# Performance work log

Hardware: AMD Instinct MI355X
Metric: run time of the kernel (lower is better)

## Reference

```python
import jax, jax.numpy as jnp
import numpy as np

K = 8  # search_range in sample_wise_recolor
BIG = 1e30


def setup_inputs() -> dict:
    key = jax.random.key(0)
    ks = jax.random.split(key, 6)
    L, N = 16384, 10000  # L: upsampled candidate voxels (multiple of 8), N: target points
    pred_F = jax.random.normal(ks[0], (L,), jnp.float32)
    cand_xyz = jax.random.normal(ks[1], (L, 3), jnp.float32) * 50.0
    cand_rgb = jax.random.uniform(ks[2], (L, 3), jnp.float32)
    tgt_xyz = jax.random.normal(ks[3], (N, 3), jnp.float32) * 50.0
    tgt_rgb = jax.random.uniform(ks[4], (N, 3), jnp.float32)
    keep_target = jax.random.randint(ks[5], (L,), 0, 2, jnp.int32)
    return {"pred_F": pred_F, "cand_xyz": cand_xyz, "cand_rgb": cand_rgb,
            "tgt_xyz": tgt_xyz, "tgt_rgb": tgt_rgb, "keep_target": keep_target,
            "points_num": 8192}


def _get_keep(pred, points_num):
    # local-max mask over groups of 8 children (scatter of per-row argmax)
    L = pred.shape[0]
    p8 = pred.reshape(-1, 8)
    rows = jnp.arange(p8.shape[0])
    is_local_max = jnp.zeros(p8.shape, dtype=bool).at[rows, jnp.argmax(p8, axis=1)].set(True).reshape(-1)
    # kthvalue over the non-local-max subset: local-max entries pushed to +inf so the
    # k-th smallest of the full sorted array equals the k-th smallest of the subset.
    k = L - points_num  # static python int
    vals = jnp.where(is_local_max, jnp.inf, pred)
    threshold = jnp.sort(vals)[k - 1]
    return (pred > threshold) | is_local_max


def _pairwise_sqdist(a, b):
    # a: [P,3], b: [Q,3] -> [P,Q] squared distances
    a2 = jnp.sum(a * a, axis=1)
    b2 = jnp.sum(b * b, axis=1)
    d2 = a2[:, None] + b2[None, :] - 2.0 * (a @ b.T)
    return jnp.maximum(d2, 0.0)


def _recolor_loss(cand_xyz, rgb, keep, tgt_xyz, tgt_rgb):
    L = cand_xyz.shape[0]
    N = tgt_xyz.shape[0]
    d2 = _pairwise_sqdist(tgt_xyz, cand_xyz)  # [N, L]

    # ---- recolor_backward: KNN from each target point into kept candidates ----
    d_masked = jnp.where(keep[None, :], d2, BIG)
    neg_d, idx = jax.lax.top_k(-d_masked, K)  # [N, K]
    d = -neg_d
    zero_mask = d == 0.0
    min_mask = (d == jnp.min(d, axis=1, keepdims=True)) & ~jnp.any(zero_mask, axis=1)[:, None]
    w = jnp.where(min_mask, 1.0 / jnp.sqrt(jnp.maximum(d, 1e-30)), 0.0)  # [N, K]

    flat_idx = idx.reshape(-1)
    num = jnp.zeros((L, 3), rgb.dtype).at[flat_idx].add((tgt_rgb[:, None, :] * w[:, :, None]).reshape(-1, 3))
    den = jnp.zeros((L,), rgb.dtype).at[flat_idx].add(w.reshape(-1))
    has_den = den != 0.0
    recolored = jnp.where(has_den[:, None], num / jnp.where(has_den, den, 1.0)[:, None], 0.0)

    # exact-match (zero-distance) targets overwrite; scatter with safe out-of-range dummy row
    safe_idx = jnp.where(zero_mask, idx, L).reshape(-1)
    tgt_exp = jnp.broadcast_to(tgt_rgb[:, None, :], (N, K, 3)).reshape(-1, 3)
    recolored = jnp.concatenate([recolored, jnp.zeros((1, 3), rgb.dtype)], 0).at[safe_idx].set(tgt_exp)[:L]
    empty = jnp.concatenate([~has_den, jnp.zeros((1,), bool)], 0).at[safe_idx].set(False)[:L]
    empty = empty & keep  # only kept candidates matter

    # ---- recolor_forward: kept candidates with no color yet pull from nearest targets ----
    neg_df, idxf = jax.lax.top_k(-d2.T, K)  # [L, K]
    df = -neg_df
    mf = df == jnp.min(df, axis=1, keepdims=True)
    rec_fwd = jnp.sum(tgt_rgb[idxf] * mf[:, :, None], axis=1) / jnp.sum(mf, axis=1, keepdims=True).astype(rgb.dtype)
    recolored = jnp.where(empty[:, None], rec_fwd, recolored)

    # L1 loss over kept candidates only; recolor target is no-grad in the original
    recolored = jax.lax.stop_gradient(recolored)
    return jnp.sum(jnp.where(keep[:, None], jnp.abs(rgb - recolored), 0.0))


def reference(pred_F, cand_xyz, cand_rgb, tgt_xyz, tgt_rgb, keep_target, points_num):
    keep = _get_keep(jax.lax.stop_gradient(pred_F), points_num)  # @torch.no_grad
    # coord recon loss: BCE-with-logits, reduction='sum'
    t = keep_target.astype(pred_F.dtype)
    coord_loss = jnp.sum(jnp.maximum(pred_F, 0.0) - pred_F * t + jnp.log1p(jnp.exp(-jnp.abs(pred_F))))
    # inverse_transform_for_color in training mode: x * 255
    rgb = cand_rgb * 255.0
    rgb_loss = _recolor_loss(cand_xyz, rgb, keep, tgt_xyz, tgt_rgb)
    return jnp.stack([coord_loss, rgb_loss])
```

## Files before the change

kernel.cpp:

```cpp
#include <hip/hip_runtime.h>
#include <hip/hip_bf16.h>


#define SCAN_T 256
#define BCH 512
#define FCH 512

__global__ __launch_bounds__(256) void k_init(
    const float* __restrict__ txyz, float4* __restrict__ ttile,
    float4* __restrict__ numden, int* __restrict__ zerohit,
    unsigned long long* __restrict__ tmin, unsigned long long* __restrict__ fmin,
    unsigned int* __restrict__ ghist, int* __restrict__ counters,
    float* __restrict__ out, int L, int N) {
  int i = blockIdx.x * 256 + threadIdx.x;
  if (i < N) {
    float x = txyz[3*i], y = txyz[3*i+1], z = txyz[3*i+2];
    ttile[i] = make_float4(x, y, z, fmaf(x, x, fmaf(y, y, z * z)));
    tmin[i] = ~0ull;
  }
  if (i < L) {
    numden[i] = make_float4(0.f, 0.f, 0.f, 0.f);
    zerohit[i] = 0;
    fmin[i] = ~0ull;
  }
  if (i < 2048) ghist[i] = 0u;
  if (i < 8) counters[i] = 0;
  if (i < 2) out[i] = 0.f;
}

__global__ __launch_bounds__(256) void k_prep(
    const float* __restrict__ pred, unsigned int* __restrict__ key,
    unsigned char* __restrict__ islm, unsigned int* __restrict__ ghist, int L) {
  __shared__ float sp[256];
  __shared__ unsigned char fl[256];
  __shared__ unsigned int lh[2048];
  int tid = threadIdx.x;
  int i = blockIdx.x * 256 + tid;
  sp[tid] = (i < L) ? pred[i] : -3e38f;
  fl[tid] = 0;
  for (int b = tid; b < 2048; b += 256) lh[b] = 0u;
  __syncthreads();
  if (tid < 32) {
    int base = tid * 8;
    float bv = sp[base]; int bi = 0;
    #pragma unroll
    for (int j = 1; j < 8; ++j) {
      float v = sp[base + j];
      if (v > bv) { bv = v; bi = j; }
    }
    fl[base + bi] = 1;
  }
  __syncthreads();
  if (i < L) {
    unsigned char lm = fl[tid];
    unsigned int fb = __float_as_uint(sp[tid]);
    unsigned int k = lm ? 0xFF800000u
                        : ((fb & 0x80000000u) ? ~fb : (fb | 0x80000000u));
    key[i] = k;
    islm[i] = lm;
    atomicAdd(&lh[k >> 21], 1u);
  }
  __syncthreads();
  for (int b = tid; b < 2048; b += 256) {
    unsigned int c = lh[b];
    if (c) atomicAdd(&ghist[b], c);
  }
}

__global__ __launch_bounds__(256) void k_sel(
    const unsigned int* __restrict__ key, const unsigned int* __restrict__ ghist,
    const int* __restrict__ pnum_p, float* __restrict__ thr_out, int L) {
  __shared__ unsigned int buf[16384];
  __shared__ unsigned int hist[256];
  __shared__ unsigned int sB, sR, sM;
  int tid = threadIdx.x;
  unsigned int rank = (unsigned int)(L - pnum_p[0] - 1);
  if (tid == 0) sM = 0u;
  if (tid < 64) {
    unsigned int sum = 0;
    #pragma unroll 4
    for (int j = 0; j < 32; ++j) sum += ghist[tid * 32 + j];
    unsigned int incl = sum;
    for (int o = 1; o < 64; o <<= 1) {
      unsigned int v = __shfl_up(incl, o);
      if (tid >= o) incl += v;
    }
    unsigned int excl = incl - sum;
    bool cond = (rank >= excl) && (rank < incl);
    unsigned long long bal = __ballot(cond);
    int first = __ffsll((long long)bal) - 1;
    if (tid == first) {
      unsigned int r = rank - excl, cum = 0;
      for (int j = 0; j < 32; ++j) {
        unsigned int c = ghist[tid * 32 + j];
        if (r < cum + c) { sB = (unsigned int)(tid * 32 + j); sR = r - cum; break; }
        cum += c;
      }
    }
  }
  __syncthreads();
  unsigned int B = sB;
  for (int i = tid; i < L; i += 256) {
    unsigned int k = key[i];
    if ((k >> 21) == B) { unsigned int p = atomicAdd(&sM, 1u); buf[p] = k; }
  }
  __syncthreads();
  unsigned int M = sM;
  unsigned int pfx = B << 21;
  const int shifts[3] = {13, 5, 0};
  const unsigned int masks[3] = {0xFFE00000u, 0xFFFFE000u, 0xFFFFFFE0u};
  const int nbs[3] = {256, 256, 32};
  for (int p = 0; p < 3; ++p) {
    hist[tid & 255] = 0u;
    __syncthreads();
    unsigned int mk = masks[p]; int sh = shifts[p]; int nb = nbs[p];
    unsigned int pm = pfx & mk;
    for (unsigned int j = tid; j < M; j += 256) {
      unsigned int k = buf[j];
      if ((k & mk) == pm) atomicAdd(&hist[(k >> sh) & (unsigned)(nb - 1)], 1u);
    }
    __syncthreads();
    if (tid < 64) {
      int g = nb >> 6; if (g < 1) g = 1;
      unsigned int sum = 0;
      for (int j = 0; j < g; ++j) {
        int idx = tid * g + j;
        if (idx < nb) sum += hist[idx];
      }
      unsigned int incl = sum;
      for (int o = 1; o < 64; o <<= 1) {
        unsigned int v = __shfl_up(incl, o);
        if (tid >= o) incl += v;
      }
      unsigned int excl = incl - sum;
      unsigned int r = sR;
      bool cond = (r >= excl) && (r < incl);
      unsigned long long bal = __ballot(cond);
      int first = __ffsll((long long)bal) - 1;
      if (tid == first) {
        unsigned int rr = r - excl, cum = 0;
        for (int j = 0; j < g; ++j) {
          int idx = tid * g + j;
          if (idx >= nb) break;
          unsigned int c = hist[idx];
          if (rr < cum + c) { sB = (unsigned int)idx; sR = rr - cum; break; }
          cum += c;
        }
      }
    }
    __syncthreads();
    pfx |= sB << sh;
    __syncthreads();
  }
  if (tid == 0) {
    unsigned int kk = pfx;
    unsigned int fb = (kk & 0x80000000u) ? (kk & 0x7FFFFFFFu) : ~kk;
    thr_out[0] = __uint_as_float(fb);
  }
}

__global__ __launch_bounds__(256) void k_keepc(
    const float* __restrict__ pred, const unsigned char* __restrict__ islm,
    const float* __restrict__ thr_p, const float* __restrict__ cxyz,
    const int* __restrict__ ktgt, int* __restrict__ keep,
    float4* __restrict__ klist, int* __restrict__ kidx,
    int* __restrict__ counters, float* __restrict__ out, int L) {
  int i = blockIdx.x * 256 + threadIdx.x;
  float thr = thr_p[0];
  float term = 0.f;
  if (i < L) {
    float p = pred[i];
    bool kp = (p > thr) || islm[i];
    keep[i] = kp ? 1 : 0;
    if (kp) {
      int pos = atomicAdd(&counters[0], 1);
      float x = cxyz[3*i], y = cxyz[3*i+1], z = cxyz[3*i+2];
      klist[pos] = make_float4(x, y, z, fmaf(x, x, fmaf(y, y, z * z)));
      kidx[pos] = i;
    }
    float t = (float)ktgt[i];
    term = fmaxf(p, 0.f) - p * t + log1pf(expf(-fabsf(p)));
  }
  for (int off = 32; off > 0; off >>= 1) term += __shfl_down(term, off);
  if ((threadIdx.x & 63) == 0) atomicAdd(&out[0], term);
}

__global__ __launch_bounds__(SCAN_T) void k_bwd(
    const float* __restrict__ txyz, const float4* __restrict__ klist,
    const int* __restrict__ kidx, const int* __restrict__ counters,
    unsigned long long* __restrict__ tmin, int N) {
  int kc = counters[0];
  int c0 = blockIdx.y * BCH;
  if (c0 >= kc) return;
  int c1 = min(c0 + BCH, kc);
  __shared__ float4 sc[SCAN_T];
  int tid = threadIdx.x;
  int t = blockIdx.x * SCAN_T + tid;
  float tx = 0.f, ty = 0.f, tz = 0.f;
  if (t < N) { tx = txyz[3*t]; ty = txyz[3*t+1]; tz = txyz[3*t+2]; }
  float ntx = -2.f * tx, nty = -2.f * ty, ntz = -2.f * tz;
  float best = 3e38f; int bpos = -1;
  for (int tile = c0; tile < c1; tile += SCAN_T) {
    int cnt = min(SCAN_T, c1 - tile);
    if (tid < cnt) sc[tid] = klist[tile + tid];
    __syncthreads();
    #pragma unroll 8
    for (int c = 0; c < cnt; ++c) {
      float4 cd = sc[c];
      float d = fmaf(ntx, cd.x, cd.w);
      d = fmaf(nty, cd.y, d);
      d = fmaf(ntz, cd.z, d);
      if (d < best) { best = d; bpos = tile + c; }
    }
    __syncthreads();
  }
  if (t < N && bpos >= 0) {
    float4 cd = klist[bpos];
    float dx = tx - cd.x, dy = ty - cd.y, dz = tz - cd.z;
    float dtrue = fmaf(dx, dx, fmaf(dy, dy, dz * dz));
    unsigned long long pack =
        ((unsigned long long)__float_as_uint(dtrue) << 32) |
        (unsigned int)kidx[bpos];
    atomicMin(&tmin[t], pack);
  }
}

__global__ __launch_bounds__(256) void k_bwd_scatter(
    const float* __restrict__ trgb, const unsigned long long* __restrict__ tmin,
    float4* __restrict__ numden, int* __restrict__ zerohit,
    float4* __restrict__ zcolor, int N) {
  int t = blockIdx.x * 256 + threadIdx.x;
  if (t >= N) return;
  unsigned long long pack = tmin[t];
  float d = __uint_as_float((unsigned int)(pack >> 32));
  int idx = (int)(pack & 0xFFFFFFFFull);
  float r = trgb[3*t], g = trgb[3*t+1], b = trgb[3*t+2];
  if (d == 0.0f) {
    zerohit[idx] = 1;
    zcolor[idx] = make_float4(r, g, b, 0.f);
  } else {
    float w = 1.0f / sqrtf(fmaxf(d, 1e-30f));
    atomicAdd(&numden[idx].x, r * w);
    atomicAdd(&numden[idx].y, g * w);
    atomicAdd(&numden[idx].z, b * w);
    atomicAdd(&numden[idx].w, w);
  }
}

__global__ __launch_bounds__(256) void k_empty(
    const int* __restrict__ keep, const float4* __restrict__ numden,
    const int* __restrict__ zerohit, int* __restrict__ elist,
    int* __restrict__ counters, int L) {
  int l = blockIdx.x * 256 + threadIdx.x;
  if (l < L && keep[l] && (numden[l].w == 0.f) && (zerohit[l] == 0)) {
    int pos = atomicAdd(&counters[1], 1);
    elist[pos] = l;
  }
}

__global__ __launch_bounds__(SCAN_T) void k_fwd(
    const float4* __restrict__ ttile, const float* __restrict__ cxyz,
    const int* __restrict__ elist, const int* __restrict__ counters,
    unsigned long long* __restrict__ fmin, int N) {
  int ec = counters[1];
  if ((int)(blockIdx.x * SCAN_T) >= ec) return;
  __shared__ float4 st[SCAN_T];
  int tid = threadIdx.x;
  int e = blockIdx.x * SCAN_T + tid;
  bool act = e < ec;
  int l = act ? elist[e] : 0;
  float cx = 0.f, cy = 0.f, cz = 0.f;
  if (act) { cx = cxyz[3*l]; cy = cxyz[3*l+1]; cz = cxyz[3*l+2]; }
  float ncx = -2.f * cx, ncy = -2.f * cy, ncz = -2.f * cz;
  float c2 = fmaf(cx, cx, fmaf(cy, cy, cz * cz));
  int t0 = blockIdx.y * FCH;
  int t1 = min(t0 + FCH, N);
  float best = 3e38f; int bidx = 0;
  for (int tile = t0; tile < t1; tile += SCAN_T) {
    int cnt = min(SCAN_T, t1 - tile);
    if (tid < cnt) st[tid] = ttile[tile + tid];
    __syncthreads();
    #pragma unroll 8
    for (int c = 0; c < cnt; ++c) {
      float4 td = st[c];
      float d = fmaf(ncx, td.x, td.w);
      d = fmaf(ncy, td.y, d);
      d = fmaf(ncz, td.z, d);
      if (d < best) { best = d; bidx = tile + c; }
    }
    __syncthreads();
  }
  if (act) {
    float dkey = fmaxf(best + c2, 0.f);
    unsigned long long pack =
        ((unsigned long long)__float_as_uint(dkey) << 32) | (unsigned int)bidx;
    atomicMin(&fmin[l], pack);
  }
}

__global__ __launch_bounds__(256) void k_loss(
    const float* __restrict__ crgb, const float* __restrict__ trgb,
    const int* __restrict__ keep, const float4* __restrict__ numden,
    const int* __restrict__ zerohit, const float4* __restrict__ zcolor,
    const unsigned long long* __restrict__ fmin,
    float* __restrict__ out, int L) {
  int l = blockIdx.x * 256 + threadIdx.x;
  float loss = 0.f;
  if (l < L && keep[l]) {
    float rr, rg, rb;
    if (zerohit[l]) {
      float4 z = zcolor[l]; rr = z.x; rg = z.y; rb = z.z;
    } else {
      float4 nd = numden[l];
      if (nd.w != 0.f) { rr = nd.x / nd.w; rg = nd.y / nd.w; rb = nd.z / nd.w; }
      else {
        int ti = (int)(fmin[l] & 0xFFFFFFFFull);
        rr = trgb[3*ti]; rg = trgb[3*ti+1]; rb = trgb[3*ti+2];
      }
    }
    float sr = crgb[3*l] * 255.f, sg = crgb[3*l+1] * 255.f, sb = crgb[3*l+2] * 255.f;
    loss = fabsf(sr - rr) + fabsf(sg - rg) + fabsf(sb - rb);
  }
  for (int off = 32; off > 0; off >>= 1) loss += __shfl_down(loss, off);
  if ((threadIdx.x & 63) == 0) atomicAdd(&out[1], loss);
}

extern "C" void kernel_launch(void* const* d_in, const int* in_sizes, int n_in,
                              void* d_out, int out_size, void* d_ws, size_t ws_size,
                              hipStream_t stream) {
  const float* pred = (const float*)d_in[0];
  const float* cxyz = (const float*)d_in[1];
  const float* crgb = (const float*)d_in[2];
  const float* txyz = (const float*)d_in[3];
  const float* trgb = (const float*)d_in[4];
  const int*   ktgt = (const int*)d_in[5];
  const int*   pnum = (const int*)d_in[6];
  int L = in_sizes[0];
  int N = in_sizes[3] / 3;

  char* ws = (char*)d_ws;
  size_t off = 0;
  int* keep = (int*)(ws + off);                      off += (size_t)L * 4;
  float4* klist = (float4*)(ws + off);               off += (size_t)L * 16;
  int* kidx = (int*)(ws + off);                      off += (size_t)L * 4;
  float4* ttile = (float4*)(ws + off);               off += (size_t)((N + 3) & ~3) * 16;
  float4* numden = (float4*)(ws + off);              off += (size_t)L * 16;
  int* zerohit = (int*)(ws + off);                   off += (size_t)L * 4;
  float4* zcolor = (float4*)(ws + off);              off += (size_t)L * 16;
  unsigned long long* tmin = (unsigned long long*)(ws + off); off += (size_t)((N + 1) & ~1) * 8;
  unsigned long long* fmin = (unsigned long long*)(ws + off); off += (size_t)L * 8;
  int* elist = (int*)(ws + off);                     off += (size_t)L * 4;
  unsigned int* key = (unsigned int*)(ws + off);     off += (size_t)L * 4;
  unsigned char* islm = (unsigned char*)(ws + off);  off += ((size_t)L + 15) & ~15ull;
  unsigned int* ghist = (unsigned int*)(ws + off);   off += 2048 * 4;
  float* thr_slot = (float*)(ws + off);              off += 16;
  int* counters = (int*)(ws + off);                  off += 256;

  float* out = (float*)d_out;
  int mx = max(L, N);
  int nbL = (L + 255) / 256;

  k_init<<<(mx + 255) / 256, 256, 0, stream>>>(
      txyz, ttile, numden, zerohit, tmin, fmin, ghist, counters, out, L, N);

  k_prep<<<nbL, 256, 0, stream>>>(pred, key, islm, ghist, L);

  k_sel<<<1, 256, 0, stream>>>(key, ghist, pnum, thr_slot, L);

  k_keepc<<<nbL, 256, 0, stream>>>(
      pred, islm, thr_slot, cxyz, ktgt, keep, klist, kidx, counters, out, L);

  dim3 g2((N + SCAN_T - 1) / SCAN_T, (L + BCH - 1) / BCH);
  k_bwd<<<g2, SCAN_T, 0, stream>>>(txyz, klist, kidx, counters, tmin, N);

  k_bwd_scatter<<<(N + 255) / 256, 256, 0, stream>>>(
      trgb, tmin, numden, zerohit, zcolor, N);

  k_empty<<<nbL, 256, 0, stream>>>(keep, numden, zerohit, elist, counters, L);

  dim3 g3((L + SCAN_T - 1) / SCAN_T, (N + FCH - 1) / FCH);
  k_fwd<<<g3, SCAN_T, 0, stream>>>(ttile, cxyz, elist, counters, fmin, N);

  k_loss<<<(L + 255) / 256, 256, 0, stream>>>(
      crgb, trgb, keep, numden, zerohit, zcolor, fmin, out, L);
}
```

Measured before the change: 164.2 us.

## Fuse all pipeline stages into one cooperative persistent kernel with grid syncs

Replaces the nine separate kernel launches with a single cooperative kernel of 256 blocks that moves between stages using grid.sync(). This removes per-launch overhead and inter-kernel gaps. It also vectorizes the local-max and key preparation to one thread per group of 8 with global histogram atomics, parallelizes the radix-select bucket gather across the grid, and splits the NN scans into fixed chunk tasks. The cost is reduced parallelism in the scan phases, since only 256 blocks run, plus the latency of each grid barrier. Contention on global atomics also rises because the block-local histogram is gone.

```diff
diff --git a/kernel.cpp b/kernel.cpp
--- a/kernel.cpp
+++ b/kernel.cpp
@@ -1,89 +1,82 @@
 #include <hip/hip_runtime.h>
+#include <hip/hip_cooperative_groups.h>
 #include <hip/hip_bf16.h>
 
-
-#define SCAN_T 256
-#define BCH 512
-#define FCH 512
-
-__global__ __launch_bounds__(256) void k_init(
-    const float* __restrict__ txyz, float4* __restrict__ ttile,
-    float4* __restrict__ numden, int* __restrict__ zerohit,
-    unsigned long long* __restrict__ tmin, unsigned long long* __restrict__ fmin,
-    unsigned int* __restrict__ ghist, int* __restrict__ counters,
-    float* __restrict__ out, int L, int N) {
-  int i = blockIdx.x * 256 + threadIdx.x;
-  if (i < N) {
-    float x = txyz[3*i], y = txyz[3*i+1], z = txyz[3*i+2];
-    ttile[i] = make_float4(x, y, z, fmaf(x, x, fmaf(y, y, z * z)));
-    tmin[i] = ~0ull;
-  }
-  if (i < L) {
-    numden[i] = make_float4(0.f, 0.f, 0.f, 0.f);
-    zerohit[i] = 0;
-    fmin[i] = ~0ull;
-  }
-  if (i < 2048) ghist[i] = 0u;
-  if (i < 8) counters[i] = 0;
-  if (i < 2) out[i] = 0.f;
-}
-
-__global__ __launch_bounds__(256) void k_prep(
-    const float* __restrict__ pred, unsigned int* __restrict__ key,
-    unsigned char* __restrict__ islm, unsigned int* __restrict__ ghist, int L) {
-  __shared__ float sp[256];
-  __shared__ unsigned char fl[256];
-  __shared__ unsigned int lh[2048];
-  int tid = threadIdx.x;
-  int i = blockIdx.x * 256 + tid;
-  sp[tid] = (i < L) ? pred[i] : -3e38f;
-  fl[tid] = 0;
-  for (int b = tid; b < 2048; b += 256) lh[b] = 0u;
-  __syncthreads();
-  if (tid < 32) {
-    int base = tid * 8;
-    float bv = sp[base]; int bi = 0;
+namespace cg = cooperative_groups;
+
+
+#define NBLK 256
+#define NTHR 256
+
+struct Params {
+  const float* pred; const float* cxyz; const float* crgb;
+  const float* txyz; const float* trgb; const int* ktgt; const int* pnum;
+  float4* klist; float4* ttile; float4* numden; float4* zcolor;
+  unsigned long long* tmin; unsigned long long* fmin;
+  int* keep; int* kidx; int* zerohit; int* elist;
+  unsigned int* key; unsigned int* ghist; unsigned int* gbuf;
+  float* thr_slot; int* counters; unsigned char* islm;
+  float* out; int L; int N;
+};
+
+__global__ __launch_bounds__(NTHR, 1) void k_all(Params p) {
+  cg::grid_group grid = cg::this_grid();
+  __shared__ float4 tile[256];
+  __shared__ unsigned int hist[256];
+  __shared__ unsigned int buf[16384];
+  __shared__ unsigned int sB, sR;
+  int tid = threadIdx.x, bid = blockIdx.x;
+  int gidx = bid * NTHR + tid;
+  int gsz = (int)gridDim.x * NTHR;
+  int L = p.L, N = p.N;
+
+  for (int i = gidx; i < N; i += gsz) {
+    float x = p.txyz[3*i], y = p.txyz[3*i+1], z = p.txyz[3*i+2];
+    p.ttile[i] = make_float4(x, y, z, fmaf(x, x, fmaf(y, y, z * z)));
+    p.tmin[i] = ~0ull;
+  }
+  for (int i = gidx; i < L; i += gsz) {
+    p.numden[i] = make_float4(0.f, 0.f, 0.f, 0.f);
+    p.zerohit[i] = 0;
+    p.fmin[i] = ~0ull;
+  }
+  if (gidx < 2048) p.ghist[gidx] = 0u;
+  if (gidx < 8) p.counters[gidx] = 0;
+  if (gidx < 2) p.out[gidx] = 0.f;
+  grid.sync();
+
+  int ngroups = L >> 3;
+  for (int g = gidx; g < ngroups; g += gsz) {
+    const float4* pv = (const float4*)p.pred + (size_t)g * 2;
+    float4 a = pv[0], b = pv[1];
+    float v[8] = {a.x, a.y, a.z, a.w, b.x, b.y, b.z, b.w};
+    int bi = 0; float bv = v[0];
     #pragma unroll
-    for (int j = 1; j < 8; ++j) {
-      float v = sp[base + j];
-      if (v > bv) { bv = v; bi = j; }
-    }
-    fl[base + bi] = 1;
-  }
-  __syncthreads();
-  if (i < L) {
-    unsigned char lm = fl[tid];
-    unsigned int fb = __float_as_uint(sp[tid]);
-    unsigned int k = lm ? 0xFF800000u
-                        : ((fb & 0x80000000u) ? ~fb : (fb | 0x80000000u));
-    key[i] = k;
-    islm[i] = lm;
-    atomicAdd(&lh[k >> 21], 1u);
-  }
-  __syncthreads();
-  for (int b = tid; b < 2048; b += 256) {
-    unsigned int c = lh[b];
-    if (c) atomicAdd(&ghist[b], c);
-  }
-}
-
-__global__ __launch_bounds__(256) void k_sel(
-    const unsigned int* __restrict__ key, const unsigned int* __restrict__ ghist,
-    const int* __restrict__ pnum_p, float* __restrict__ thr_out, int L) {
-  __shared__ unsigned int buf[16384];
-  __shared__ unsigned int hist[256];
-  __shared__ unsigned int sB, sR, sM;
-  int tid = threadIdx.x;
-  unsigned int rank = (unsigned int)(L - pnum_p[0] - 1);
-  if (tid == 0) sM = 0u;
+    for (int j = 1; j < 8; ++j) if (v[j] > bv) { bv = v[j]; bi = j; }
+    unsigned int kk[8];
+    unsigned long long lmpack = 0ull;
+    #pragma unroll
+    for (int j = 0; j < 8; ++j) {
+      unsigned int fb = __float_as_uint(v[j]);
+      unsigned int mk = (fb & 0x80000000u) ? ~fb : (fb | 0x80000000u);
+      if (j == bi) { mk = 0xFF800000u; lmpack |= 1ull << (8 * j); }
+      kk[j] = mk;
+      atomicAdd(&p.ghist[mk >> 21], 1u);
+    }
+    ((uint4*)p.key)[g*2]   = make_uint4(kk[0], kk[1], kk[2], kk[3]);
+    ((uint4*)p.key)[g*2+1] = make_uint4(kk[4], kk[5], kk[6], kk[7]);
+    *(unsigned long long*)(p.islm + (size_t)g * 8) = lmpack;
+  }
+  grid.sync();
+
+  unsigned int rank = (unsigned int)(L - p.pnum[0] - 1);
   if (tid < 64) {
     unsigned int sum = 0;
-    #pragma unroll 4
-    for (int j = 0; j < 32; ++j) sum += ghist[tid * 32 + j];
+    for (int j = 0; j < 32; ++j) sum += p.ghist[tid * 32 + j];
     unsigned int incl = sum;
     for (int o = 1; o < 64; o <<= 1) {
-      unsigned int v = __shfl_up(incl, o);
-      if (tid >= o) incl += v;
+      unsigned int vv = __shfl_up(incl, o);
+      if (tid >= o) incl += vv;
     }
     unsigned int excl = incl - sum;
     bool cond = (rank >= excl) && (rank < incl);
@@ -92,7 +85,7 @@
     if (tid == first) {
       unsigned int r = rank - excl, cum = 0;
       for (int j = 0; j < 32; ++j) {
-        unsigned int c = ghist[tid * 32 + j];
+        unsigned int c = p.ghist[tid * 32 + j];
         if (r < cum + c) { sB = (unsigned int)(tid * 32 + j); sR = r - cum; break; }
         cum += c;
       }
@@ -100,287 +93,256 @@
   }
   __syncthreads();
   unsigned int B = sB;
-  for (int i = tid; i < L; i += 256) {
-    unsigned int k = key[i];
-    if ((k >> 21) == B) { unsigned int p = atomicAdd(&sM, 1u); buf[p] = k; }
-  }
-  __syncthreads();
-  unsigned int M = sM;
-  unsigned int pfx = B << 21;
-  const int shifts[3] = {13, 5, 0};
-  const unsigned int masks[3] = {0xFFE00000u, 0xFFFFE000u, 0xFFFFFFE0u};
-  const int nbs[3] = {256, 256, 32};
-  for (int p = 0; p < 3; ++p) {
-    hist[tid & 255] = 0u;
+  for (int i = gidx; i < L; i += gsz) {
+    unsigned int k = p.key[i];
+    if ((k >> 21) == B) {
+      unsigned int pos = atomicAdd((unsigned int*)&p.counters[2], 1u);
+      p.gbuf[pos] = k;
+    }
+  }
+  grid.sync();
+
+  if (bid == 0) {
+    unsigned int M = (unsigned int)p.counters[2];
+    for (unsigned int j = tid; j < M; j += NTHR) buf[j] = p.gbuf[j];
     __syncthreads();
-    unsigned int mk = masks[p]; int sh = shifts[p]; int nb = nbs[p];
-    unsigned int pm = pfx & mk;
-    for (unsigned int j = tid; j < M; j += 256) {
-      unsigned int k = buf[j];
-      if ((k & mk) == pm) atomicAdd(&hist[(k >> sh) & (unsigned)(nb - 1)], 1u);
-    }
-    __syncthreads();
-    if (tid < 64) {
-      int g = nb >> 6; if (g < 1) g = 1;
-      unsigned int sum = 0;
-      for (int j = 0; j < g; ++j) {
-        int idx = tid * g + j;
-        if (idx < nb) sum += hist[idx];
-      }
-      unsigned int incl = sum;
-      for (int o = 1; o < 64; o <<= 1) {
-        unsigned int v = __shfl_up(incl, o);
-        if (tid >= o) incl += v;
-      }
-      unsigned int excl = incl - sum;
-      unsigned int r = sR;
-      bool cond = (r >= excl) && (r < incl);
-      unsigned long long bal = __ballot(cond);
-      int first = __ffsll((long long)bal) - 1;
-      if (tid == first) {
-        unsigned int rr = r - excl, cum = 0;
-        for (int j = 0; j < g; ++j) {
-          int idx = tid * g + j;
-          if (idx >= nb) break;
-          unsigned int c = hist[idx];
-          if (rr < cum + c) { sB = (unsigned int)idx; sR = rr - cum; break; }
-          cum += c;
-        }
-      }
-    }
-    __syncthreads();
-    pfx |= sB << sh;
-    __syncthreads();
-  }
-  if (tid == 0) {
-    unsigned int kk = pfx;
-    unsigned int fb = (kk & 0x80000000u) ? (kk & 0x7FFFFFFFu) : ~kk;
-    thr_out[0] = __uint_as_float(fb);
-  }
-}
-
-__global__ __launch_bounds__(256) void k_keepc(
-    const float* __restrict__ pred, const unsigned char* __restrict__ islm,
-    const float* __restrict__ thr_p, const float* __restrict__ cxyz,
-    const int* __restrict__ ktgt, int* __restrict__ keep,
-    float4* __restrict__ klist, int* __restrict__ kidx,
-    int* __restrict__ counters, float* __restrict__ out, int L) {
-  int i = blockIdx.x * 256 + threadIdx.x;
-  float thr = thr_p[0];
-  float term = 0.f;
-  if (i < L) {
-    float p = pred[i];
-    bool kp = (p > thr) || islm[i];
-    keep[i] = kp ? 1 : 0;
-    if (kp) {
-      int pos = atomicAdd(&counters[0], 1);
-      float x = cxyz[3*i], y = cxyz[3*i+1], z = cxyz[3*i+2];
-      klist[pos] = make_float4(x, y, z, fmaf(x, x, fmaf(y, y, z * z)));
-      kidx[pos] = i;
-    }
-    float t = (float)ktgt[i];
-    term = fmaxf(p, 0.f) - p * t + log1pf(expf(-fabsf(p)));
-  }
-  for (int off = 32; off > 0; off >>= 1) term += __shfl_down(term, off);
-  if ((threadIdx.x & 63) == 0) atomicAdd(&out[0], term);
-}
-
-__global__ __launch_bounds__(SCAN_T) void k_bwd(
-    const float* __restrict__ txyz, const float4* __restrict__ klist,
-    const int* __restrict__ kidx, const int* __restrict__ counters,
-    unsigned long long* __restrict__ tmin, int N) {
-  int kc = counters[0];
-  int c0 = blockIdx.y * BCH;
-  if (c0 >= kc) return;
-  int c1 = min(c0 + BCH, kc);
-  __shared__ float4 sc[SCAN_T];
-  int tid = threadIdx.x;
-  int t = blockIdx.x * SCAN_T + tid;
-  float tx = 0.f, ty = 0.f, tz = 0.f;
-  if (t < N) { tx = txyz[3*t]; ty = txyz[3*t+1]; tz = txyz[3*t+2]; }
-  float ntx = -2.f * tx, nty = -2.f * ty, ntz = -2.f * tz;
-  float best = 3e38f; int bpos = -1;
-  for (int tile = c0; tile < c1; tile += SCAN_T) {
-    int cnt = min(SCAN_T, c1 - tile);
-    if (tid < cnt) sc[tid] = klist[tile + tid];
-    __syncthreads();
-    #pragma unroll 8
-    for (int c = 0; c < cnt; ++c) {
-      float4 cd = sc[c];
-      float d = fmaf(ntx, cd.x, cd.w);
-      d = fmaf(nty, cd.y, d);
-      d = fmaf(ntz, cd.z, d);
-      if (d < best) { best = d; bpos = tile + c; }
-    }
-    __syncthreads();
-  }
-  if (t < N && bpos >= 0) {
-    float4 cd = klist[bpos];
-    float dx = tx - cd.x, dy = ty - cd.y, dz = tz - cd.z;
-    float dtrue = fmaf(dx, dx, fmaf(dy, dy, dz * dz));
-    unsigned long long pack =
-        ((unsigned long long)__float_as_uint(dtrue) << 32) |
-        (unsigned int)kidx[bpos];
-    atomicMin(&tmin[t], pack);
-  }
-}
-
-__global__ __launch_bounds__(256) void k_bwd_scatter(
-    const float* __restrict__ trgb, const unsigned long long* __restrict__ tmin,
-    float4* __restrict__ numden, int* __restrict__ zerohit,
-    float4* __restrict__ zcolor, int N) {
-  int t = blockIdx.x * 256 + threadIdx.x;
-  if (t >= N) return;
-  unsigned long long pack = tmin[t];
-  float d = __uint_as_float((unsigned int)(pack >> 32));
-  int idx = (int)(pack & 0xFFFFFFFFull);
-  float r = trgb[3*t], g = trgb[3*t+1], b = trgb[3*t+2];
-  if (d == 0.0f) {
-    zerohit[idx] = 1;
-    zcolor[idx] = make_float4(r, g, b, 0.f);
-  } else {
-    float w = 1.0f / sqrtf(fmaxf(d, 1e-30f));
-    atomicAdd(&numden[idx].x, r * w);
-    atomicAdd(&numden[idx].y, g * w);
-    atomicAdd(&numden[idx].z, b * w);
-    atomicAdd(&numden[idx].w, w);
-  }
-}
-
-__global__ __launch_bounds__(256) void k_empty(
-    const int* __restrict__ keep, const float4* __restrict__ numden,
-    const int* __restrict__ zerohit, int* __restrict__ elist,
-    int* __restrict__ counters, int L) {
-  int l = blockIdx.x * 256 + threadIdx.x;
-  if (l < L && keep[l] && (numden[l].w == 0.f) && (zerohit[l] == 0)) {
-    int pos = atomicAdd(&counters[1], 1);
-    elist[pos] = l;
-  }
-}
-
-__global__ __launch_bounds__(SCAN_T) void k_fwd(
-    const float4* __restrict__ ttile, const float* __restrict__ cxyz,
-    const int* __restrict__ elist, const int* __restrict__ counters,
-    unsigned long long* __restrict__ fmin, int N) {
-  int ec = counters[1];
-  if ((int)(blockIdx.x * SCAN_T) >= ec) return;
-  __shared__ float4 st[SCAN_T];
-  int tid = threadIdx.x;
-  int e = blockIdx.x * SCAN_T + tid;
-  bool act = e < ec;
-  int l = act ? elist[e] : 0;
-  float cx = 0.f, cy = 0.f, cz = 0.f;
-  if (act) { cx = cxyz[3*l]; cy = cxyz[3*l+1]; cz = cxyz[3*l+2]; }
-  float ncx = -2.f * cx, ncy = -2.f * cy, ncz = -2.f * cz;
-  float c2 = fmaf(cx, cx, fmaf(cy, cy, cz * cz));
-  int t0 = blockIdx.y * FCH;
-  int t1 = min(t0 + FCH, N);
-  float best = 3e38f; int bidx = 0;
-  for (int tile = t0; tile < t1; tile += SCAN_T) {
-    int cnt = min(SCAN_T, t1 - tile);
-    if (tid < cnt) st[tid] = ttile[tile + tid];
-    __syncthreads();
-    #pragma unroll 8
-    for (int c = 0; c < cnt; ++c) {
-      float4 td = st[c];
-      float d = fmaf(ncx, td.x, td.w);
-      d = fmaf(ncy, td.y, d);
-      d = fmaf(ncz, td.z, d);
-      if (d < best) { best = d; bidx = tile + c; }
-    }
-    __syncthreads();
-  }
-  if (act) {
-    float dkey = fmaxf(best + c2, 0.f);
-    unsigned long long pack =
-        ((unsigned long long)__float_as_uint(dkey) << 32) | (unsigned int)bidx;
-    atomicMin(&fmin[l], pack);
-  }
-}
-
-__global__ __launch_bounds__(256) void k_loss(
-    const float* __restrict__ crgb, const float* __restrict__ trgb,
-    const int* __restrict__ keep, const float4* __restrict__ numden,
-    const int* __restrict__ zerohit, const float4* __restrict__ zcolor,
-    const unsigned long long* __restrict__ fmin,
-    float* __restrict__ out, int L) {
-  int l = blockIdx.x * 256 + threadIdx.x;
-  float loss = 0.f;
-  if (l < L && keep[l]) {
-    float rr, rg, rb;
-    if (zerohit[l]) {
-      float4 z = zcolor[l]; rr = z.x; rg = z.y; rb = z.z;
+    unsigned int pfx = B << 21;
+    const int shifts[3] = {13, 5, 0};
+    const unsigned int masks[3] = {0xFFE00000u, 0xFFFFE000u, 0xFFFFFFE0u};
+    const int nbs[3] = {256, 256, 32};
+    for (int pass = 0; pass < 3; ++pass) {
+      hist[tid] = 0u;
+      __syncthreads();
+      unsigned int mk = masks[pass]; int sh = shifts[pass]; int nb = nbs[pass];
+      unsigned int pm = pfx & mk;
+      for (unsigned int j = tid; j < M; j += NTHR) {
+        unsigned int k = buf[j];
+        if ((k & mk) == pm) atomicAdd(&hist[(k >> sh) & (unsigned)(nb - 1)], 1u);
+      }
+      __syncthreads();
+      if (tid < 64) {
+        int g = nb >> 6; if (g < 1) g = 1;
+        unsigned int sum = 0;
+        for (int j = 0; j < g; ++j) { int idx = tid * g + j; if (idx < nb) sum += hist[idx]; }
+        unsigned int incl = sum;
+        for (int o = 1; o < 64; o <<= 1) {
+          unsigned int vv = __shfl_up(incl, o);
+          if (tid >= o) incl += vv;
+        }
+        unsigned int excl = incl - sum;
+        unsigned int r = sR;
+        bool cond = (r >= excl) && (r < incl);
+        unsigned long long bal = __ballot(cond);
+        int first = __ffsll((long long)bal) - 1;
+        if (tid == first) {
+          unsigned int rr = r - excl, cum = 0;
+          for (int j = 0; j < g; ++j) {
+            int idx = tid * g + j; if (idx >= nb) break;
+            unsigned int c = hist[idx];
+            if (rr < cum + c) { sB = (unsigned int)idx; sR = rr - cum; break; }
+            cum += c;
+          }
+        }
+      }
+      __syncthreads();
+      pfx |= sB << sh;
+      __syncthreads();
+    }
+    if (tid == 0) {
+      unsigned int kk2 = pfx;
+      unsigned int fb = (kk2 & 0x80000000u) ? (kk2 & 0x7FFFFFFFu) : ~kk2;
+      p.thr_slot[0] = __uint_as_float(fb);
+    }
+  }
+  grid.sync();
+
+  {
+    float thr = p.thr_slot[0];
+    float term = 0.f;
+    for (int i = gidx; i < L; i += gsz) {
+      float v = p.pred[i];
+      bool kp = (v > thr) || p.islm[i];
+      p.keep[i] = kp ? 1 : 0;
+      if (kp) {
+        int pos = atomicAdd(&p.counters[0], 1);
+        float x = p.cxyz[3*i], y = p.cxyz[3*i+1], z = p.cxyz[3*i+2];
+        p.klist[pos] = make_float4(x, y, z, fmaf(x, x, fmaf(y, y, z * z)));
+        p.kidx[pos] = i;
+      }
+      float t = (float)p.ktgt[i];
+      term += fmaxf(v, 0.f) - v * t + log1pf(expf(-fabsf(v)));
+    }
+    for (int o = 32; o > 0; o >>= 1) term += __shfl_down(term, o);
+    if ((tid & 63) == 0) atomicAdd(&p.out[0], term);
+  }
+  grid.sync();
+
+  {
+    int kc = p.counters[0];
+    int ntb = (N + 255) / 256;
+    const int NC = 6;
+    int csz = ((kc + NC - 1) / NC + 255) & ~255;
+    for (int task = bid; task < ntb * NC; task += (int)gridDim.x) {
+      int tb = task / NC, cb = task % NC;
+      int c0 = cb * csz, c1 = min(c0 + csz, kc);
+      int t = tb * 256 + tid;
+      bool act = t < N;
+      float tx = 0.f, ty = 0.f, tz = 0.f;
+      if (act) { tx = p.txyz[3*t]; ty = p.txyz[3*t+1]; tz = p.txyz[3*t+2]; }
+      float ntx = -2.f * tx, nty = -2.f * ty, ntz = -2.f * tz;
+      float best = 3e38f; int bpos = -1;
+      for (int tb0 = c0; tb0 < c1; tb0 += 256) {
+        int cnt = min(256, c1 - tb0);
+        __syncthreads();
+        if (tid < cnt) tile[tid] = p.klist[tb0 + tid];
+        __syncthreads();
+        #pragma unroll 8
+        for (int c = 0; c < cnt; ++c) {
+          float4 cd = tile[c];
+          float d = fmaf(ntx, cd.x, cd.w);
+          d = fmaf(nty, cd.y, d);
+          d = fmaf(ntz, cd.z, d);
+          if (d < best) { best = d; bpos = tb0 + c; }
+        }
+      }
+      if (act && bpos >= 0) {
+        float4 cd = p.klist[bpos];
+        float dx = tx - cd.x, dy = ty - cd.y, dz = tz - cd.z;
+        float dtrue = fmaf(dx, dx, fmaf(dy, dy, dz * dz));
+        unsigned long long pack =
+            ((unsigned long long)__float_as_uint(dtrue) << 32) |
+            (unsigned int)p.kidx[bpos];
+        atomicMin(&p.tmin[t], pack);
+      }
+    }
+  }
+  grid.sync();
+
+  for (int t = gidx; t < N; t += gsz) {
+    unsigned long long pack = p.tmin[t];
+    float d = __uint_as_float((unsigned int)(pack >> 32));
+    int idx = (int)(pack & 0xFFFFFFFFull);
+    float r = p.trgb[3*t], g2 = p.trgb[3*t+1], b2 = p.trgb[3*t+2];
+    if (d == 0.0f) {
+      p.zerohit[idx] = 1;
+      p.zcolor[idx] = make_float4(r, g2, b2, 0.f);
     } else {
-      float4 nd = numden[l];
-      if (nd.w != 0.f) { rr = nd.x / nd.w; rg = nd.y / nd.w; rb = nd.z / nd.w; }
-      else {
-        int ti = (int)(fmin[l] & 0xFFFFFFFFull);
-        rr = trgb[3*ti]; rg = trgb[3*ti+1]; rb = trgb[3*ti+2];
-      }
-    }
-    float sr = crgb[3*l] * 255.f, sg = crgb[3*l+1] * 255.f, sb = crgb[3*l+2] * 255.f;
-    loss = fabsf(sr - rr) + fabsf(sg - rg) + fabsf(sb - rb);
-  }
-  for (int off = 32; off > 0; off >>= 1) loss += __shfl_down(loss, off);
-  if ((threadIdx.x & 63) == 0) atomicAdd(&out[1], loss);
+      float w = 1.0f / sqrtf(fmaxf(d, 1e-30f));
+      atomicAdd(&p.numden[idx].x, r * w);
+      atomicAdd(&p.numden[idx].y, g2 * w);
+      atomicAdd(&p.numden[idx].z, b2 * w);
+      atomicAdd(&p.numden[idx].w, w);
+    }
+  }
+  grid.sync();
+
+  for (int l = gidx; l < L; l += gsz) {
+    if (p.keep[l] && (p.numden[l].w == 0.f) && (p.zerohit[l] == 0)) {
+      int pos = atomicAdd(&p.counters[1], 1);
+      p.elist[pos] = l;
+    }
+  }
+  grid.sync();
+
+  {
+    int ec = p.counters[1];
+    int neb = (ec + 255) / 256;
+    const int NTC = 5;
+    int tcs = ((N + NTC - 1) / NTC + 255) & ~255;
+    for (int task = bid; task < neb * NTC; task += (int)gridDim.x) {
+      int eb = task / NTC, tc = task % NTC;
+      int t0 = tc * tcs, t1 = min(t0 + tcs, N);
+      int e = eb * 256 + tid;
+      bool act = e < ec;
+      int l = act ? p.elist[e] : 0;
+      float cx = 0.f, cy = 0.f, cz = 0.f;
+      if (act) { cx = p.cxyz[3*l]; cy = p.cxyz[3*l+1]; cz = p.cxyz[3*l+2]; }
+      float ncx = -2.f * cx, ncy = -2.f * cy, ncz = -2.f * cz;
+      float c2 = fmaf(cx, cx, fmaf(cy, cy, cz * cz));
+      float best = 3e38f; int bx = 0;
+      for (int tb0 = t0; tb0 < t1; tb0 += 256) {
+        int cnt = min(256, t1 - tb0);
+        __syncthreads();
+        if (tid < cnt) tile[tid] = p.ttile[tb0 + tid];
+        __syncthreads();
+        #pragma unroll 8
+        for (int c = 0; c < cnt; ++c) {
+          float4 td = tile[c];
+          float d = fmaf(ncx, td.x, td.w);
+          d = fmaf(ncy, td.y, d);
+          d = fmaf(ncz, td.z, d);
+          if (d < best) { best = d; bx = tb0 + c; }
+        }
+      }
+      if (act) {
+        float dkey = fmaxf(best + c2, 0.f);
+        unsigned long long pack =
+            ((unsigned long long)__float_as_uint(dkey) << 32) | (unsigned int)bx;
+        atomicMin(&p.fmin[l], pack);
+      }
+    }
+  }
+  grid.sync();
+
+  {
+    float loss = 0.f;
+    for (int l = gidx; l < L; l += gsz) {
+      if (p.keep[l]) {
+        float rr, rg, rb;
+        if (p.zerohit[l]) {
+          float4 z = p.zcolor[l]; rr = z.x; rg = z.y; rb = z.z;
+        } else {
+          float4 nd = p.numden[l];
+          if (nd.w != 0.f) { rr = nd.x / nd.w; rg = nd.y / nd.w; rb = nd.z / nd.w; }
+          else {
+            int ti = (int)(p.fmin[l] & 0xFFFFFFFFull);
+            rr = p.trgb[3*ti]; rg = p.trgb[3*ti+1]; rb = p.trgb[3*ti+2];
+          }
+        }
+        float sr = p.crgb[3*l]*255.f, sg = p.crgb[3*l+1]*255.f, sb = p.crgb[3*l+2]*255.f;
+        loss += fabsf(sr - rr) + fabsf(sg - rg) + fabsf(sb - rb);
+      }
+    }
+    for (int o = 32; o > 0; o >>= 1) loss += __shfl_down(loss, o);
+    if ((tid & 63) == 0) atomicAdd(&p.out[1], loss);
+  }
 }
 
 extern "C" void kernel_launch(void* const* d_in, const int* in_sizes, int n_in,
                               void* d_out, int out_size, void* d_ws, size_t ws_size,
                               hipStream_t stream) {
-  const float* pred = (const float*)d_in[0];
-  const float* cxyz = (const float*)d_in[1];
-  const float* crgb = (const float*)d_in[2];
-  const float* txyz = (const float*)d_in[3];
-  const float* trgb = (const float*)d_in[4];
-  const int*   ktgt = (const int*)d_in[5];
-  const int*   pnum = (const int*)d_in[6];
+  Params prm;
+  prm.pred = (const float*)d_in[0];
+  prm.cxyz = (const float*)d_in[1];
+  prm.crgb = (const float*)d_in[2];
+  prm.txyz = (const float*)d_in[3];
+  prm.trgb = (const float*)d_in[4];
+  prm.ktgt = (const int*)d_in[5];
+  prm.pnum = (const int*)d_in[6];
   int L = in_sizes[0];
   int N = in_sizes[3] / 3;
+  prm.L = L; prm.N = N;
 
   char* ws = (char*)d_ws;
   size_t off = 0;
-  int* keep = (int*)(ws + off);                      off += (size_t)L * 4;
-  float4* klist = (float4*)(ws + off);               off += (size_t)L * 16;
-  int* kidx = (int*)(ws + off);                      off += (size_t)L * 4;
-  float4* ttile = (float4*)(ws + off);               off += (size_t)((N + 3) & ~3) * 16;
-  float4* numden = (float4*)(ws + off);              off += (size_t)L * 16;
-  int* zerohit = (int*)(ws + off);                   off += (size_t)L * 4;
-  float4* zcolor = (float4*)(ws + off);              off += (size_t)L * 16;
-  unsigned long long* tmin = (unsigned long long*)(ws + off); off += (size_t)((N + 1) & ~1) * 8;
-  unsigned long long* fmin = (unsigned long long*)(ws + off); off += (size_t)L * 8;
-  int* elist = (int*)(ws + off);                     off += (size_t)L * 4;
-  unsigned int* key = (unsigned int*)(ws + off);     off += (size_t)L * 4;
-  unsigned char* islm = (unsigned char*)(ws + off);  off += ((size_t)L + 15) & ~15ull;
-  unsigned int* ghist = (unsigned int*)(ws + off);   off += 2048 * 4;
-  float* thr_slot = (float*)(ws + off);              off += 16;
-  int* counters = (int*)(ws + off);                  off += 256;
-
-  float* out = (float*)d_out;
-  int mx = max(L, N);
-  int nbL = (L + 255) / 256;
-
-  k_init<<<(mx + 255) / 256, 256, 0, stream>>>(
-      txyz, ttile, numden, zerohit, tmin, fmin, ghist, counters, out, L, N);
-
-  k_prep<<<nbL, 256, 0, stream>>>(pred, key, islm, ghist, L);
-
-  k_sel<<<1, 256, 0, stream>>>(key, ghist, pnum, thr_slot, L);
-
-  k_keepc<<<nbL, 256, 0, stream>>>(
-      pred, islm, thr_slot, cxyz, ktgt, keep, klist, kidx, counters, out, L);
-
-  dim3 g2((N + SCAN_T - 1) / SCAN_T, (L + BCH - 1) / BCH);
-  k_bwd<<<g2, SCAN_T, 0, stream>>>(txyz, klist, kidx, counters, tmin, N);
-
-  k_bwd_scatter<<<(N + 255) / 256, 256, 0, stream>>>(
-      trgb, tmin, numden, zerohit, zcolor, N);
-
-  k_empty<<<nbL, 256, 0, stream>>>(keep, numden, zerohit, elist, counters, L);
-
-  dim3 g3((L + SCAN_T - 1) / SCAN_T, (N + FCH - 1) / FCH);
-  k_fwd<<<g3, SCAN_T, 0, stream>>>(ttile, cxyz, elist, counters, fmin, N);
-
-  k_loss<<<(L + 255) / 256, 256, 0, stream>>>(
-      crgb, trgb, keep, numden, zerohit, zcolor, fmin, out, L);
+  prm.klist  = (float4*)(ws + off);             off += (size_t)L * 16;
+  prm.ttile  = (float4*)(ws + off);             off += (size_t)((N + 3) & ~3) * 16;
+  prm.numden = (float4*)(ws + off);             off += (size_t)L * 16;
+  prm.zcolor = (float4*)(ws + off);             off += (size_t)L * 16;
+  prm.tmin   = (unsigned long long*)(ws + off); off += (size_t)((N + 1) & ~1) * 8;
+  prm.fmin   = (unsigned long long*)(ws + off); off += (size_t)L * 8;
+  prm.keep   = (int*)(ws + off);                off += (size_t)L * 4;
+  prm.kidx   = (int*)(ws + off);                off += (size_t)L * 4;
+  prm.zerohit= (int*)(ws + off);                off += (size_t)L * 4;
+  prm.elist  = (int*)(ws + off);                off += (size_t)L * 4;
+  prm.key    = (unsigned int*)(ws + off);       off += (size_t)L * 4;
+  prm.gbuf   = (unsigned int*)(ws + off);       off += (size_t)L * 4;
+  prm.ghist  = (unsigned int*)(ws + off);       off += 2048 * 4;
+  prm.thr_slot = (float*)(ws + off);            off += 16;
+  prm.counters = (int*)(ws + off);              off += 256;
+  prm.islm   = (unsigned char*)(ws + off);      off += ((size_t)L + 15) & ~15ull;
+  prm.out    = (float*)d_out;
+
+  void* args[] = {&prm};
+  hipLaunchCooperativeKernel((void*)k_all, dim3(NBLK), dim3(NTHR), args, 0, stream);
 }
```

Result: slower. 439.4 us (+167.6%).
